# Kernel tuning notes

Measured on AMD Instinct MI355X. Metric: run time of the kernel, lower is better.

Reference implementation:

```python
import jax, jax.numpy as jnp
import numpy as np

B, C, IN_F = 8, 1024, 256
NH, OF = 8, 128  # num_heads, out_features
TEMP = 1.5
LN_EPS = 1e-5


def setup_inputs() -> dict:
    key = jax.random.key(0)
    ks = jax.random.split(key, 8)
    H = jax.random.normal(ks[0], (B, C, IN_F), dtype=jnp.float32)
    A = jax.random.uniform(ks[1], (B, C, C), dtype=jnp.float32)
    W = jax.random.normal(ks[2], (IN_F, NH * OF), dtype=jnp.float32) * 0.05
    a = jax.random.normal(ks[3], (NH, 2 * OF), dtype=jnp.float32) * 0.05
    res_W = jax.random.normal(ks[4], (IN_F, NH * OF), dtype=jnp.float32) * 0.05
    res_b = jnp.zeros((NH * OF,), dtype=jnp.float32)
    ln_gamma = jnp.ones((NH * OF,), dtype=jnp.float32)
    ln_beta = jnp.zeros((NH * OF,), dtype=jnp.float32)
    return {"H": H, "A": A, "W": W, "a": a, "res_W": res_W,
            "res_b": res_b, "ln_gamma": ln_gamma, "ln_beta": ln_beta}


def reference(H, A, W, a, res_W, res_b, ln_gamma, ln_beta):
    b, c, _ = H.shape
    # Wh: [B, C, H, F]
    Wh = (H @ W).reshape(b, c, NH, OF)
    # Split attention vector a = [a_src | a_dst] so that
    # einsum('bijhf,hf', cat(Wh_i, Wh_j), a) == e_src[i] + e_dst[j]
    a_src, a_dst = a[:, :OF], a[:, OF:]
    e_src = jnp.einsum('bchf,hf->bch', Wh, a_src)  # [B, C, H]
    e_dst = jnp.einsum('bchf,hf->bch', Wh, a_dst)  # [B, C, H]
    e = e_src[:, :, None, :] + e_dst[:, None, :, :]  # [B, C, C, H]
    e = jnp.where(e > 0, e, 0.2 * e)  # LeakyReLU(0.2)
    # adjacency mask with self-loops
    mask = (A > 0) | jnp.eye(c, dtype=bool)[None]  # [B, C, C]
    e = jnp.where(mask[..., None], e, -1e9)
    # row-normalized adjacency as additive bias
    A_norm = A / (A.sum(axis=-1, keepdims=True) + 1e-8)
    e = e + A_norm[..., None]
    alpha = jax.nn.softmax(e / TEMP, axis=2)  # softmax over j (dim=2)
    # dropout disabled (inference / p-effective 0)
    H_out = jnp.einsum('bijh,bjhf->bihf', alpha, Wh).reshape(b, c, NH * OF)
    x = H_out + (H @ res_W + res_b)
    mu = x.mean(axis=-1, keepdims=True)
    var = x.var(axis=-1, keepdims=True)
    x = (x - mu) * jax.lax.rsqrt(var + LN_EPS) * ln_gamma + ln_beta
    return jax.nn.relu(x), alpha
```

## Files before the change

### kernel.cpp

```cpp
#include <hip/hip_runtime.h>

#define BB 8
#define CC 1024
#define FF 256
#define NHH 8
#define OFF 128
#define NHOF 1024
#define KSCALE 0.9617966939259756f

typedef __attribute__((ext_vector_type(8))) short s8v;
typedef __attribute__((ext_vector_type(4))) short s4v;
typedef __attribute__((ext_vector_type(4))) float f32x4;
typedef __attribute__((ext_vector_type(16))) float f32x16;

__device__ __forceinline__ ushort f2b(float f) {
  union { float f; uint u; } v; v.f = f;
  uint r = v.u + 0x7FFFu + ((v.u >> 16) & 1u);
  return (ushort)(r >> 16);
}

__global__ __launch_bounds__(256) void k_prep(const float* __restrict__ W,
    const float* __restrict__ RW, short* __restrict__ Wt, short* __restrict__ RWt)
{
  __shared__ float st[32][33];
  const float* src = blockIdx.z ? RW : W;
  short* dst = blockIdx.z ? RWt : Wt;
  const int n0 = blockIdx.x * 32, k0 = blockIdx.y * 32;
  const int t = threadIdx.x;
  {
    int kr = t >> 3, nq = (t & 7) * 4;
    float4 v = *reinterpret_cast<const float4*>(src + (size_t)(k0 + kr) * NHOF + n0 + nq);
    st[kr][nq] = v.x; st[kr][nq + 1] = v.y; st[kr][nq + 2] = v.z; st[kr][nq + 3] = v.w;
  }
  __syncthreads();
  {
    int nr = t >> 3, kq = (t & 7) * 4;
    s4v pk;
    pk[0] = (short)f2b(st[kq + 0][nr]); pk[1] = (short)f2b(st[kq + 1][nr]);
    pk[2] = (short)f2b(st[kq + 2][nr]); pk[3] = (short)f2b(st[kq + 3][nr]);
    *reinterpret_cast<s4v*>(dst + (size_t)(n0 + nr) * FF + k0 + kq) = pk;
  }
}

__global__ __launch_bounds__(256) void k_gemm(const float* __restrict__ H,
    const short* __restrict__ Wt, const short* __restrict__ RWt,
    const float* __restrict__ rb, const float* __restrict__ att,
    short* __restrict__ WhT, float* __restrict__ Rs,
    float* __restrict__ esg, float* __restrict__ edg)
{
  __shared__ short SU[8192];
  __shared__ float ep[2][128][2];
  short* As = SU;
  short* Bs = SU + 4096;
  const int t = threadIdx.x, l = t & 63, w = t >> 6;
  const int wr = w >> 1, wc = w & 1;
  const int nb = blockIdx.x, m0 = blockIdx.y * 128;
  const bool isW = nb < 8;
  const int n0 = (nb & 7) * 128;
  const short* Bg = isW ? Wt : RWt;

  f32x4 acc[4][4];
#pragma unroll
  for (int mi = 0; mi < 4; ++mi)
#pragma unroll
    for (int ni = 0; ni < 4; ++ni)
#pragma unroll
      for (int r = 0; r < 4; ++r) acc[mi][ni][r] = 0.f;

  const int srow = t >> 1, skh = (t & 1) * 16;
  const float* hsrc = H + (size_t)(m0 + srow) * FF + skh;
  const short* bsrc = Bg + (size_t)(n0 + srow) * FF + skh;
  const int fr = l & 15, kg = (l >> 4) * 8;

  for (int k0 = 0; k0 < FF; k0 += 32) {
    float4 h0 = *reinterpret_cast<const float4*>(hsrc + k0);
    float4 h1 = *reinterpret_cast<const float4*>(hsrc + k0 + 4);
    float4 h2 = *reinterpret_cast<const float4*>(hsrc + k0 + 8);
    float4 h3 = *reinterpret_cast<const float4*>(hsrc + k0 + 12);
    s8v b0 = *reinterpret_cast<const s8v*>(bsrc + k0);
    s8v b1 = *reinterpret_cast<const s8v*>(bsrc + k0 + 8);
    s8v p0, p1;
    p0[0] = (short)f2b(h0.x); p0[1] = (short)f2b(h0.y); p0[2] = (short)f2b(h0.z); p0[3] = (short)f2b(h0.w);
    p0[4] = (short)f2b(h1.x); p0[5] = (short)f2b(h1.y); p0[6] = (short)f2b(h1.z); p0[7] = (short)f2b(h1.w);
    p1[0] = (short)f2b(h2.x); p1[1] = (short)f2b(h2.y); p1[2] = (short)f2b(h2.z); p1[3] = (short)f2b(h2.w);
    p1[4] = (short)f2b(h3.x); p1[5] = (short)f2b(h3.y); p1[6] = (short)f2b(h3.z); p1[7] = (short)f2b(h3.w);
    *reinterpret_cast<s8v*>(As + srow * 32 + skh) = p0;
    *reinterpret_cast<s8v*>(As + srow * 32 + skh + 8) = p1;
    *reinterpret_cast<s8v*>(Bs + srow * 32 + skh) = b0;
    *reinterpret_cast<s8v*>(Bs + srow * 32 + skh + 8) = b1;
    __syncthreads();
    s8v aF[4], bF[4];
#pragma unroll
    for (int mi = 0; mi < 4; ++mi)
      aF[mi] = *reinterpret_cast<const s8v*>(As + (wr * 64 + mi * 16 + fr) * 32 + kg);
#pragma unroll
    for (int ni = 0; ni < 4; ++ni)
      bF[ni] = *reinterpret_cast<const s8v*>(Bs + (wc * 64 + ni * 16 + fr) * 32 + kg);
#pragma unroll
    for (int mi = 0; mi < 4; ++mi)
#pragma unroll
      for (int ni = 0; ni < 4; ++ni)
        acc[mi][ni] = __builtin_amdgcn_mfma_f32_16x16x32_bf16(aF[mi], bF[ni], acc[mi][ni], 0, 0, 0);
    __syncthreads();
  }

  const int bb = m0 >> 10, jl0 = m0 & 1023;
  if (isW) {
    const int h = nb;
    float aS[4], aD[4];
#pragma unroll
    for (int ni = 0; ni < 4; ++ni) {
      int f = wc * 64 + ni * 16 + (l & 15);
      aS[ni] = att[h * 256 + f];
      aD[ni] = att[h * 256 + 128 + f];
    }
#pragma unroll
    for (int mi = 0; mi < 4; ++mi)
#pragma unroll
      for (int r = 0; r < 4; ++r) {
        float ps = acc[mi][0][r] * aS[0] + acc[mi][1][r] * aS[1] + acc[mi][2][r] * aS[2] + acc[mi][3][r] * aS[3];
        float pd = acc[mi][0][r] * aD[0] + acc[mi][1][r] * aD[1] + acc[mi][2][r] * aD[2] + acc[mi][3][r] * aD[3];
#pragma unroll
        for (int m = 1; m <= 8; m <<= 1) { ps += __shfl_xor(ps, m); pd += __shfl_xor(pd, m); }
        if ((l & 15) == 0) {
          int row = wr * 64 + mi * 16 + (l >> 4) * 4 + r;
          ep[wc][row][0] = ps; ep[wc][row][1] = pd;
        }
      }
#pragma unroll
    for (int c = 0; c < 4; ++c) {
      if (wc == (c >> 1)) {
        const int nia = (c & 1) * 2;
#pragma unroll
        for (int mi = 0; mi < 4; ++mi)
#pragma unroll
          for (int nq = 0; nq < 2; ++nq) {
            const int ni = nia + nq;
            const int f_loc = nq * 16 + (l & 15);
            const int jloc = wr * 64 + mi * 16 + (l >> 4) * 4;
            s4v pk;
            pk[0] = (short)f2b(acc[mi][ni][0]); pk[1] = (short)f2b(acc[mi][ni][1]);
            pk[2] = (short)f2b(acc[mi][ni][2]); pk[3] = (short)f2b(acc[mi][ni][3]);
            *reinterpret_cast<s4v*>(SU + f_loc * 136 + jloc) = pk;
          }
      }
      __syncthreads();
      {
        const int f_loc = t >> 3, jq = t & 7;
        s8v v0 = *reinterpret_cast<const s8v*>(SU + f_loc * 136 + jq * 16);
        s8v v1 = *reinterpret_cast<const s8v*>(SU + f_loc * 136 + jq * 16 + 8);
        short* dst = WhT + (size_t)((bb * 8 + h) * 128 + c * 32 + f_loc) * 1024 + jl0 + jq * 16;
        *reinterpret_cast<s8v*>(dst) = v0;
        *reinterpret_cast<s8v*>(dst + 8) = v1;
      }
      __syncthreads();
    }
    {
      int row = t >> 1, sel = t & 1;
      float v = ep[0][row][sel] + ep[1][row][sel];
      float* dst = sel ? edg : esg;
      dst[(size_t)((bb << 10) + jl0 + row) * 8 + h] = v;
    }
  } else {
#pragma unroll
    for (int mi = 0; mi < 4; ++mi)
#pragma unroll
      for (int ni = 0; ni < 4; ++ni) {
        int n = n0 + wc * 64 + ni * 16 + (l & 15);
        float bias = rb[n];
        int m = m0 + wr * 64 + mi * 16 + (l >> 4) * 4;
#pragma unroll
        for (int r = 0; r < 4; ++r)
          Rs[(size_t)(m + r) * NHOF + n] = acc[mi][ni][r] + bias;
      }
  }
}

__global__ __launch_bounds__(1024) void k_attn(const float* __restrict__ A,
    const short* __restrict__ WhT, const float* __restrict__ esg,
    const float* __restrict__ edg, float* __restrict__ alp, float* __restrict__ ho)
{
  __shared__ short alSf[2 * 8 * 32 * 32];
  __shared__ float edKT[1024 * 8];
  __shared__ float esK[32 * 8];
  __shared__ float liS[32 * 8];
  __shared__ float rsS[32];

  const int t = threadIdx.x, l = t & 63, w = t >> 6;
  const int b = blockIdx.x >> 5, i0 = (blockIdx.x & 31) << 5;

#pragma unroll
  for (int c = 0; c < 8; ++c) {
    int idx = t + c * 1024;
    edKT[idx] = edg[(size_t)b * 8192 + idx] * KSCALE;
  }
  if (t < 256) esK[t] = esg[(size_t)((b << 10) + i0 + (t >> 3)) * 8 + (t & 7)] * KSCALE;

  const int i = t >> 5, jsub = t & 31;
  const float* Ar = A + (size_t)((b << 10) + i0 + i) * 1024;

  {
    float s = 0.f;
#pragma unroll
    for (int c = 0; c < 8; ++c) {
      float4 v = *reinterpret_cast<const float4*>(Ar + jsub * 4 + c * 128);
      s += v.x + v.y + v.z + v.w;
    }
    s += __shfl_xor(s, 1); s += __shfl_xor(s, 2); s += __shfl_xor(s, 4);
    s += __shfl_xor(s, 8); s += __shfl_xor(s, 16);
    if (jsub == 0) rsS[i] = 1.f / (s + 1e-8f);
  }
  __syncthreads();

  {
    const int ig = i0 + i;
    const float rs = rsS[i];
    float eK[8];
#pragma unroll
    for (int h2 = 0; h2 < 8; ++h2) eK[h2] = esK[i * 8 + h2];
    float lac = 0.f;
    float lach[8] = {0, 0, 0, 0, 0, 0, 0, 0};
    (void)lac;
    for (int jj = 0; jj < 32; ++jj) {
      int j = jsub + jj * 32;
      float aij = Ar[j];
      float ea = (aij > 0.f || j == ig) ? exp2f(aij * rs * KSCALE) : 0.f;
      float4 e0 = *reinterpret_cast<const float4*>(edKT + j * 8);
      float4 e1 = *reinterpret_cast<const float4*>(edKT + j * 8 + 4);
      float ed[8] = {e0.x, e0.y, e0.z, e0.w, e1.x, e1.y, e1.z, e1.w};
#pragma unroll
      for (int h2 = 0; h2 < 8; ++h2) {
        float s = eK[h2] + ed[h2];
        s = fmaxf(s, 0.2f * s);
        lach[h2] = fmaf(exp2f(s), ea, lach[h2]);
      }
    }
#pragma unroll
    for (int h2 = 0; h2 < 8; ++h2) {
      float v = lach[h2];
      v += __shfl_xor(v, 1); v += __shfl_xor(v, 2); v += __shfl_xor(v, 4);
      v += __shfl_xor(v, 8); v += __shfl_xor(v, 16);
      if (jsub == 0) liS[i * 8 + h2] = 1.f / v;
    }
  }
  __syncthreads();

  const int ip = i, jp = jsub, igP = i0 + ip;
  const float rsP = rsS[ip];
  float eKP[8], liP[8];
#pragma unroll
  for (int h2 = 0; h2 < 8; ++h2) { eKP[h2] = esK[ip * 8 + h2]; liP[h2] = liS[ip * 8 + h2]; }
  const float* ArP = Ar;
  const int hM = w >> 1, fh = w & 1;
  const short* Wb = WhT + ((size_t)(b * 8 + hM) << 17) + (size_t)(fh * 64 + (l & 31)) * 1024 + (l >> 5) * 8;
  f32x16 acc0, acc1;
#pragma unroll
  for (int r = 0; r < 16; ++r) { acc0[r] = 0.f; acc1[r] = 0.f; }

  float areg[8];
  {
    const int j = jp;
    float aij = ArP[j];
    float ea = (aij > 0.f || j == igP) ? exp2f(aij * rsP * KSCALE) : 0.f;
    float4 e0 = *reinterpret_cast<const float4*>(edKT + j * 8);
    float4 e1 = *reinterpret_cast<const float4*>(edKT + j * 8 + 4);
    float ed[8] = {e0.x, e0.y, e0.z, e0.w, e1.x, e1.y, e1.z, e1.w};
#pragma unroll
    for (int h2 = 0; h2 < 8; ++h2) {
      float s = eKP[h2] + ed[h2];
      s = fmaxf(s, 0.2f * s);
      areg[h2] = exp2f(s) * ea * liP[h2];
    }
    float* ap = alp + (size_t)((b << 10) + igP) * 8192 + (size_t)j * 8;
    *reinterpret_cast<float4*>(ap)     = make_float4(areg[0], areg[1], areg[2], areg[3]);
    *reinterpret_cast<float4*>(ap + 4) = make_float4(areg[4], areg[5], areg[6], areg[7]);
  }

  const int swW = ((jp >> 3) ^ (ip & 3)) << 3;
  const int swR = (l & 31) & 3;
  for (int k = 0; k < 32; ++k) {
    const int buf = k & 1;
    {
      short* as = alSf + buf * 8192 + ip * 32 + swW + (jp & 7);
#pragma unroll
      for (int h2 = 0; h2 < 8; ++h2) as[h2 * 1024] = (short)f2b(areg[h2]);
    }
    __syncthreads();
    s8v bf00 = *reinterpret_cast<const s8v*>(Wb + k * 32);
    s8v bf01 = *reinterpret_cast<const s8v*>(Wb + k * 32 + 16);
    s8v bf10 = *reinterpret_cast<const s8v*>(Wb + 32768 + k * 32);
    s8v bf11 = *reinterpret_cast<const s8v*>(Wb + 32768 + k * 32 + 16);
    if (k < 31) {
      const int j = (k + 1) * 32 + jp;
      float aij = ArP[j];
      float ea = (aij > 0.f || j == igP) ? exp2f(aij * rsP * KSCALE) : 0.f;
      float4 e0 = *reinterpret_cast<const float4*>(edKT + j * 8);
      float4 e1 = *reinterpret_cast<const float4*>(edKT + j * 8 + 4);
      float ed[8] = {e0.x, e0.y, e0.z, e0.w, e1.x, e1.y, e1.z, e1.w};
#pragma unroll
      for (int h2 = 0; h2 < 8; ++h2) {
        float s = eKP[h2] + ed[h2];
        s = fmaxf(s, 0.2f * s);
        areg[h2] = exp2f(s) * ea * liP[h2];
      }
      float* ap = alp + (size_t)((b << 10) + igP) * 8192 + (size_t)j * 8;
      *reinterpret_cast<float4*>(ap)     = make_float4(areg[0], areg[1], areg[2], areg[3]);
      *reinterpret_cast<float4*>(ap + 4) = make_float4(areg[4], areg[5], areg[6], areg[7]);
    }
    const short* afp = alSf + buf * 8192 + hM * 1024 + (l & 31) * 32;
    s8v af0 = *reinterpret_cast<const s8v*>(afp + ((((l >> 5)) ^ swR) << 3));
    s8v af1 = *reinterpret_cast<const s8v*>(afp + (((2 | (l >> 5)) ^ swR) << 3));
    acc0 = __builtin_amdgcn_mfma_f32_32x32x16_bf16(af0, bf00, acc0, 0, 0, 0);
    acc0 = __builtin_amdgcn_mfma_f32_32x32x16_bf16(af1, bf01, acc0, 0, 0, 0);
    acc1 = __builtin_amdgcn_mfma_f32_32x32x16_bf16(af0, bf10, acc1, 0, 0, 0);
    acc1 = __builtin_amdgcn_mfma_f32_32x32x16_bf16(af1, bf11, acc1, 0, 0, 0);
  }

  {
    float* op = ho + (size_t)((b << 10) + i0) * 1024 + hM * 128 + fh * 64 + (l & 31);
#pragma unroll
    for (int reg = 0; reg < 16; ++reg) {
      int irow = (reg & 3) + 8 * (reg >> 2) + 4 * (l >> 5);
      op[(size_t)irow * 1024]      = acc0[reg];
      op[(size_t)irow * 1024 + 32] = acc1[reg];
    }
  }
}

__global__ __launch_bounds__(256) void k_ln(const float* __restrict__ Rs,
    const float* __restrict__ g, const float* __restrict__ bt, float* __restrict__ out)
{
  __shared__ float sm[8];
  const int row = blockIdx.x;
  const int t = threadIdx.x;
  size_t base = (size_t)row * NHOF + t * 4;
  float4 hv = *reinterpret_cast<const float4*>(out + base);
  float4 rv = *reinterpret_cast<const float4*>(Rs + base);
  float x0 = hv.x + rv.x, x1 = hv.y + rv.y, x2 = hv.z + rv.z, x3 = hv.w + rv.w;
  float s  = x0 + x1 + x2 + x3;
  float ss = x0 * x0 + x1 * x1 + x2 * x2 + x3 * x3;
#pragma unroll
  for (int m = 32; m; m >>= 1) { s += __shfl_xor(s, m); ss += __shfl_xor(ss, m); }
  if ((t & 63) == 0) { sm[t >> 6] = s; sm[4 + (t >> 6)] = ss; }
  __syncthreads();
  s  = sm[0] + sm[1] + sm[2] + sm[3];
  ss = sm[4] + sm[5] + sm[6] + sm[7];
  float mu = s * (1.f / 1024.f);
  float var = ss * (1.f / 1024.f) - mu * mu;
  float rstd = rsqrtf(var + 1e-5f);
  float4 gv = *reinterpret_cast<const float4*>(g + t * 4);
  float4 bv = *reinterpret_cast<const float4*>(bt + t * 4);
  float y0 = fmaxf((x0 - mu) * rstd * gv.x + bv.x, 0.f);
  float y1 = fmaxf((x1 - mu) * rstd * gv.y + bv.y, 0.f);
  float y2 = fmaxf((x2 - mu) * rstd * gv.z + bv.z, 0.f);
  float y3 = fmaxf((x3 - mu) * rstd * gv.w + bv.w, 0.f);
  *reinterpret_cast<float4*>(out + base) = make_float4(y0, y1, y2, y3);
}

extern "C" void kernel_launch(void* const* d_in, const int* in_sizes, int n_in,
                              void* d_out, int out_size, void* d_ws, size_t ws_size,
                              hipStream_t stream) {
  const float* H    = (const float*)d_in[0];
  const float* A    = (const float*)d_in[1];
  const float* W    = (const float*)d_in[2];
  const float* av   = (const float*)d_in[3];
  const float* resW = (const float*)d_in[4];
  const float* resb = (const float*)d_in[5];
  const float* gam  = (const float*)d_in[6];
  const float* bet  = (const float*)d_in[7];

  float* out0  = (float*)d_out;
  float* alpha = out0 + (size_t)BB * CC * NHOF;

  short* WhT = (short*)d_ws;
  float* res = (float*)(WhT + (size_t)8388608);
  float* esg = res + (size_t)8388608;
  float* edg = esg + 65536;
  short* Wtb = (short*)(edg + 65536);
  short* RWtb = Wtb + 262144;

  k_prep<<<dim3(32, 8, 2), 256, 0, stream>>>(W, resW, Wtb, RWtb);
  k_gemm<<<dim3(16, 64), 256, 0, stream>>>(H, Wtb, RWtb, resb, av, WhT, res, esg, edg);
  k_attn<<<256, 1024, 0, stream>>>(A, WhT, esg, edg, alpha, out0);
  k_ln  <<<BB * CC, 256, 0, stream>>>(res, gam, bet, out0);
}
```

Before: 484.0 us.

## Fuse LayerNorm into attention epilogue and pre-convert H to bf16 once

The residual add, LayerNorm and ReLU move into the attention kernel's epilogue. Row statistics are reduced across waves through shared memory, so the separate LN kernel and its round trip of the 32 MB output disappear. H is also converted to bf16 once in the prep kernel, so the GEMM no longer repeats the fp32 load and convert for each of its 16 column blocks. This adds an extra pass over H and some synchronisation and register pressure in the attention kernel.

Measured after the change: 478.2 us. About the same (-1.2%).

```diff
diff --git a/kernel.cpp b/kernel.cpp
--- a/kernel.cpp
+++ b/kernel.cpp
@@ -20,13 +20,26 @@
 }
 
 __global__ __launch_bounds__(256) void k_prep(const float* __restrict__ W,
-    const float* __restrict__ RW, short* __restrict__ Wt, short* __restrict__ RWt)
+    const float* __restrict__ RW, const float* __restrict__ H,
+    short* __restrict__ Wt, short* __restrict__ RWt, short* __restrict__ Hb)
 {
+  const int t = threadIdx.x;
+  if (blockIdx.z == 2) {
+    size_t base = ((size_t)(blockIdx.y * 32 + blockIdx.x)) * 8192 + t * 4;
+#pragma unroll
+    for (int c = 0; c < 8; ++c) {
+      float4 v = *reinterpret_cast<const float4*>(H + base + c * 1024);
+      s4v pk;
+      pk[0] = (short)f2b(v.x); pk[1] = (short)f2b(v.y);
+      pk[2] = (short)f2b(v.z); pk[3] = (short)f2b(v.w);
+      *reinterpret_cast<s4v*>(Hb + base + c * 1024) = pk;
+    }
+    return;
+  }
   __shared__ float st[32][33];
   const float* src = blockIdx.z ? RW : W;
   short* dst = blockIdx.z ? RWt : Wt;
   const int n0 = blockIdx.x * 32, k0 = blockIdx.y * 32;
-  const int t = threadIdx.x;
   {
     int kr = t >> 3, nq = (t & 7) * 4;
     float4 v = *reinterpret_cast<const float4*>(src + (size_t)(k0 + kr) * NHOF + n0 + nq);
@@ -42,7 +55,7 @@
   }
 }
 
-__global__ __launch_bounds__(256) void k_gemm(const float* __restrict__ H,
+__global__ __launch_bounds__(256) void k_gemm(const short* __restrict__ Hb,
     const short* __restrict__ Wt, const short* __restrict__ RWt,
     const float* __restrict__ rb, const float* __restrict__ att,
     short* __restrict__ WhT, float* __restrict__ Rs,
@@ -68,24 +81,17 @@
       for (int r = 0; r < 4; ++r) acc[mi][ni][r] = 0.f;
 
   const int srow = t >> 1, skh = (t & 1) * 16;
-  const float* hsrc = H + (size_t)(m0 + srow) * FF + skh;
+  const short* hsrc = Hb + (size_t)(m0 + srow) * FF + skh;
   const short* bsrc = Bg + (size_t)(n0 + srow) * FF + skh;
   const int fr = l & 15, kg = (l >> 4) * 8;
 
   for (int k0 = 0; k0 < FF; k0 += 32) {
-    float4 h0 = *reinterpret_cast<const float4*>(hsrc + k0);
-    float4 h1 = *reinterpret_cast<const float4*>(hsrc + k0 + 4);
-    float4 h2 = *reinterpret_cast<const float4*>(hsrc + k0 + 8);
-    float4 h3 = *reinterpret_cast<const float4*>(hsrc + k0 + 12);
+    s8v a0 = *reinterpret_cast<const s8v*>(hsrc + k0);
+    s8v a1 = *reinterpret_cast<const s8v*>(hsrc + k0 + 8);
     s8v b0 = *reinterpret_cast<const s8v*>(bsrc + k0);
     s8v b1 = *reinterpret_cast<const s8v*>(bsrc + k0 + 8);
-    s8v p0, p1;
-    p0[0] = (short)f2b(h0.x); p0[1] = (short)f2b(h0.y); p0[2] = (short)f2b(h0.z); p0[3] = (short)f2b(h0.w);
-    p0[4] = (short)f2b(h1.x); p0[5] = (short)f2b(h1.y); p0[6] = (short)f2b(h1.z); p0[7] = (short)f2b(h1.w);
-    p1[0] = (short)f2b(h2.x); p1[1] = (short)f2b(h2.y); p1[2] = (short)f2b(h2.z); p1[3] = (short)f2b(h2.w);
-    p1[4] = (short)f2b(h3.x); p1[5] = (short)f2b(h3.y); p1[6] = (short)f2b(h3.z); p1[7] = (short)f2b(h3.w);
-    *reinterpret_cast<s8v*>(As + srow * 32 + skh) = p0;
-    *reinterpret_cast<s8v*>(As + srow * 32 + skh + 8) = p1;
+    *reinterpret_cast<s8v*>(As + srow * 32 + skh) = a0;
+    *reinterpret_cast<s8v*>(As + srow * 32 + skh + 8) = a1;
     *reinterpret_cast<s8v*>(Bs + srow * 32 + skh) = b0;
     *reinterpret_cast<s8v*>(Bs + srow * 32 + skh + 8) = b1;
     __syncthreads();
@@ -178,13 +184,18 @@
 
 __global__ __launch_bounds__(1024) void k_attn(const float* __restrict__ A,
     const short* __restrict__ WhT, const float* __restrict__ esg,
-    const float* __restrict__ edg, float* __restrict__ alp, float* __restrict__ ho)
+    const float* __restrict__ edg, const float* __restrict__ res,
+    const float* __restrict__ gam, const float* __restrict__ bet,
+    float* __restrict__ alp, float* __restrict__ out0)
 {
   __shared__ short alSf[2 * 8 * 32 * 32];
   __shared__ float edKT[1024 * 8];
   __shared__ float esK[32 * 8];
   __shared__ float liS[32 * 8];
   __shared__ float rsS[32];
+  __shared__ float lnP[2][32][16];
+  __shared__ float muS[32];
+  __shared__ float sdS[32];
 
   const int t = threadIdx.x, l = t & 63, w = t >> 6;
   const int b = blockIdx.x >> 5, i0 = (blockIdx.x & 31) << 5;
@@ -218,9 +229,7 @@
     float eK[8];
 #pragma unroll
     for (int h2 = 0; h2 < 8; ++h2) eK[h2] = esK[i * 8 + h2];
-    float lac = 0.f;
     float lach[8] = {0, 0, 0, 0, 0, 0, 0, 0};
-    (void)lac;
     for (int jj = 0; jj < 32; ++jj) {
       int j = jsub + jj * 32;
       float aij = Ar[j];
@@ -317,44 +326,46 @@
   }
 
   {
-    float* op = ho + (size_t)((b << 10) + i0) * 1024 + hM * 128 + fh * 64 + (l & 31);
+    const float* rp = res + ((size_t)((b << 10) + i0)) * 1024 + hM * 128 + fh * 64 + (l & 31);
 #pragma unroll
     for (int reg = 0; reg < 16; ++reg) {
       int irow = (reg & 3) + 8 * (reg >> 2) + 4 * (l >> 5);
-      op[(size_t)irow * 1024]      = acc0[reg];
-      op[(size_t)irow * 1024 + 32] = acc1[reg];
-    }
-  }
-}
-
-__global__ __launch_bounds__(256) void k_ln(const float* __restrict__ Rs,
-    const float* __restrict__ g, const float* __restrict__ bt, float* __restrict__ out)
-{
-  __shared__ float sm[8];
-  const int row = blockIdx.x;
-  const int t = threadIdx.x;
-  size_t base = (size_t)row * NHOF + t * 4;
-  float4 hv = *reinterpret_cast<const float4*>(out + base);
-  float4 rv = *reinterpret_cast<const float4*>(Rs + base);
-  float x0 = hv.x + rv.x, x1 = hv.y + rv.y, x2 = hv.z + rv.z, x3 = hv.w + rv.w;
-  float s  = x0 + x1 + x2 + x3;
-  float ss = x0 * x0 + x1 * x1 + x2 * x2 + x3 * x3;
-#pragma unroll
-  for (int m = 32; m; m >>= 1) { s += __shfl_xor(s, m); ss += __shfl_xor(ss, m); }
-  if ((t & 63) == 0) { sm[t >> 6] = s; sm[4 + (t >> 6)] = ss; }
-  __syncthreads();
-  s  = sm[0] + sm[1] + sm[2] + sm[3];
-  ss = sm[4] + sm[5] + sm[6] + sm[7];
-  float mu = s * (1.f / 1024.f);
-  float var = ss * (1.f / 1024.f) - mu * mu;
-  float rstd = rsqrtf(var + 1e-5f);
-  float4 gv = *reinterpret_cast<const float4*>(g + t * 4);
-  float4 bv = *reinterpret_cast<const float4*>(bt + t * 4);
-  float y0 = fmaxf((x0 - mu) * rstd * gv.x + bv.x, 0.f);
-  float y1 = fmaxf((x1 - mu) * rstd * gv.y + bv.y, 0.f);
-  float y2 = fmaxf((x2 - mu) * rstd * gv.z + bv.z, 0.f);
-  float y3 = fmaxf((x3 - mu) * rstd * gv.w + bv.w, 0.f);
-  *reinterpret_cast<float4*>(out + base) = make_float4(y0, y1, y2, y3);
+      acc0[reg] += rp[(size_t)irow * 1024];
+      acc1[reg] += rp[(size_t)irow * 1024 + 32];
+      float sp = acc0[reg] + acc1[reg];
+      float sq = acc0[reg] * acc0[reg] + acc1[reg] * acc1[reg];
+#pragma unroll
+      for (int m = 1; m <= 16; m <<= 1) { sp += __shfl_xor(sp, m); sq += __shfl_xor(sq, m); }
+      if ((l & 31) == 0) { lnP[0][irow][w] = sp; lnP[1][irow][w] = sq; }
+    }
+  }
+  __syncthreads();
+  if (t < 512) {
+    int row = t >> 4, wv = t & 15;
+    float sp = lnP[0][row][wv], sq = lnP[1][row][wv];
+#pragma unroll
+    for (int m = 1; m <= 8; m <<= 1) { sp += __shfl_xor(sp, m); sq += __shfl_xor(sq, m); }
+    if (wv == 0) {
+      float mu = sp * (1.f / 1024.f);
+      float var = sq * (1.f / 1024.f) - mu * mu;
+      muS[row] = mu;
+      sdS[row] = rsqrtf(var + 1e-5f);
+    }
+  }
+  __syncthreads();
+  {
+    const int colA = hM * 128 + fh * 64 + (l & 31);
+    float g0 = gam[colA], g1 = gam[colA + 32];
+    float b0 = bet[colA], b1 = bet[colA + 32];
+    float* op = out0 + ((size_t)((b << 10) + i0)) * 1024 + colA;
+#pragma unroll
+    for (int reg = 0; reg < 16; ++reg) {
+      int irow = (reg & 3) + 8 * (reg >> 2) + 4 * (l >> 5);
+      float mu = muS[irow], rsd = sdS[irow];
+      op[(size_t)irow * 1024]      = fmaxf((acc0[reg] - mu) * rsd * g0 + b0, 0.f);
+      op[(size_t)irow * 1024 + 32] = fmaxf((acc1[reg] - mu) * rsd * g1 + b1, 0.f);
+    }
+  }
 }
 
 extern "C" void kernel_launch(void* const* d_in, const int* in_sizes, int n_in,
@@ -378,9 +389,9 @@
   float* edg = esg + 65536;
   short* Wtb = (short*)(edg + 65536);
   short* RWtb = Wtb + 262144;
-
-  k_prep<<<dim3(32, 8, 2), 256, 0, stream>>>(W, resW, Wtb, RWtb);
-  k_gemm<<<dim3(16, 64), 256, 0, stream>>>(H, Wtb, RWtb, resb, av, WhT, res, esg, edg);
-  k_attn<<<256, 1024, 0, stream>>>(A, WhT, esg, edg, alpha, out0);
-  k_ln  <<<BB * CC, 256, 0, stream>>>(res, gam, bet, out0);
-}
+  short* Hb   = RWtb + 262144;
+
+  k_prep<<<dim3(32, 8, 3), 256, 0, stream>>>(W, resW, H, Wtb, RWtb, Hb);
+  k_gemm<<<dim3(16, 64), 256, 0, stream>>>(Hb, Wtb, RWtb, resb, av, WhT, res, esg, edg);
+  k_attn<<<256, 1024, 0, stream>>>(A, WhT, esg, edg, res, gam, bet, alpha, out0);
+}
```
